# Optimization experiments

Measured on AMD Instinct MI355X. Metric: run time of the kernel, lower is better.

Reference implementation:

```python
import jax, jax.numpy as jnp
import numpy as np

HEAD_DIM = 64
NUM_HEAD = 8
NUM_CLUSTERS = 16
B, N, M = 2, 2048, 2048


def setup_inputs() -> dict:
    key = jax.random.key(0)
    ks = jax.random.split(key, 10)
    d = HEAD_DIM
    inp = {
        "Q": jax.random.normal(ks[0], (B, NUM_HEAD, N, d), jnp.float32),
        "K": jax.random.normal(ks[1], (B, NUM_HEAD, M, d), jnp.float32),
        "V": jax.random.normal(ks[2], (B, NUM_HEAD, M, d), jnp.float32),
        "mask": jnp.zeros((B, M), jnp.int32),
        "noise": jax.random.uniform(ks[3], (B, NUM_HEAD, N, M), jnp.float32),
        "emb": jax.random.normal(ks[4], (NUM_HEAD * NUM_CLUSTERS, d), jnp.float32),
        "W1": jax.random.normal(ks[5], (d, d), jnp.float32) * 0.02,
        "b1": jnp.zeros((d,), jnp.float32),
        "W2": jax.random.normal(ks[6], (d, d), jnp.float32) * 0.02,
        "b2": jnp.zeros((d,), jnp.float32),
        "W3": jax.random.normal(ks[7], (d, d), jnp.float32) * 0.02,
        "b3": jnp.zeros((d,), jnp.float32),
    }
    return inp


def _proj(x, W1, b1, W2, b2, W3, b3):
    # torch nn.Linear: y = x @ W.T + b; dropout is identity in eval mode
    x = jax.nn.relu(jnp.einsum("bhnd,ed->bhne", x, W1) + b1)
    x = jax.nn.relu(jnp.einsum("bhnd,ed->bhne", x, W2) + b2)
    return jnp.einsum("bhnd,ed->bhne", x, W3) + b3


def reference(Q, K, V, mask, noise, emb, W1, b1, W2, b2, W3, b3):
    b, h, n, d = Q.shape
    m = V.shape[2]
    k = NUM_CLUSTERS

    clusters = emb.reshape(h, k, d)                                  # [h,k,d]
    dist = jnp.einsum("hkd,hjd->hkj", clusters, clusters)            # [h,k,k]
    # softmax over the flattened k*k matrix per head
    S = jax.nn.softmax(dist.reshape(h, k * k), axis=-1).reshape(h, k, k)

    Qhat = jax.nn.sigmoid(jnp.einsum("bhnd,hkd->bhnk", _proj(Q, W1, b1, W2, b2, W3, b3), clusters))
    Khat = jax.nn.sigmoid(jnp.einsum("bhmd,hkd->bhmk", _proj(K, W1, b1, W2, b2, W3, b3), clusters))

    SK = jnp.einsum("hkj,bhmj->bhkm", S, Khat)                       # [b,h,k,m]
    expA = jnp.einsum("bhnk,bhkm->bhnm", Qhat, SK)                   # Bernoulli probs in [0,1]

    # SampleGraphSparseGraph: Bernoulli sample with straight-through gradient
    sample = (noise < expA).astype(Q.dtype)
    graph = expA + jax.lax.stop_gradient(sample - expA)

    dot = jnp.einsum("bhnd,bhmd->bhnm", Q, K) / jnp.sqrt(jnp.asarray(d, Q.dtype))
    dot = jnp.where(mask[:, None, None, :] == 1, -jnp.inf, dot)
    p = jax.nn.softmax(dot, axis=-1) * graph
    # F.normalize(p=1): x / max(||x||_1, 1e-12); p is non-negative
    attn = p / jnp.maximum(jnp.sum(p, axis=-1, keepdims=True), 1e-12)

    X = jnp.einsum("bhnm,bhmd->bhnd", attn, V)
    sparsity = jnp.sum(graph, axis=(0, -1, -2)) / (b * n * m)        # [h]
    return X, sparsity, graph, attn
```

## Files before the change

kernel.cpp:

```cpp
#include <hip/hip_runtime.h>


typedef float  f32x4 __attribute__((ext_vector_type(4)));
typedef float  f32x8 __attribute__((ext_vector_type(8)));
typedef double f64x2 __attribute__((ext_vector_type(2)));
typedef __bf16 bf16x8 __attribute__((ext_vector_type(8)));

__device__ __forceinline__ unsigned short f2bf(float f) {
  __bf16 b = (__bf16)f;
  return __builtin_bit_cast(unsigned short, b);
}

__global__ __launch_bounds__(256) void kS(const float* __restrict__ emb,
                                          double* __restrict__ wsS,
                                          float* __restrict__ wsSP) {
  __shared__ double c[16][65];
  __shared__ double red[256];
  const int t = threadIdx.x, h = blockIdx.x;
  if (t == 0) wsSP[h] = 0.f;
  for (int i = t; i < 1024; i += 256) c[i >> 6][i & 63] = (double)emb[(size_t)h * 1024 + i];
  __syncthreads();
  const int k = t >> 4, j = t & 15;
  double acc = 0.0;
  for (int d = 0; d < 64; ++d) acc += c[k][d] * c[j][d];
  red[t] = acc; __syncthreads();
  for (int s = 128; s > 0; s >>= 1) { if (t < s) red[t] = fmax(red[t], red[t + s]); __syncthreads(); }
  const double mx = red[0]; __syncthreads();
  const double e = exp(acc - mx);
  red[t] = e; __syncthreads();
  for (int s = 128; s > 0; s >>= 1) { if (t < s) red[t] += red[t + s]; __syncthreads(); }
  wsS[h * 256 + t] = e / red[0];
}

__global__ __launch_bounds__(256) void kMLP(
    const float* __restrict__ Q, const float* __restrict__ K,
    const float* __restrict__ emb,
    const float* __restrict__ W1, const float* __restrict__ b1,
    const float* __restrict__ W2, const float* __restrict__ b2,
    const float* __restrict__ W3, const float* __restrict__ b3,
    const double* __restrict__ wsS,
    double* __restrict__ QHAT, double* __restrict__ SKT) {
  __shared__ double Xt[64][65];
  __shared__ float  Wl[64][65];
  __shared__ float  bsS[64];
  __shared__ float  cl[16][65];
  __shared__ double kh[64][17];
  __shared__ double Sl[256];

  const int t = threadIdx.x;
  const int blk = blockIdx.x;
  const int side = blk >> 9;
  const int idx = blk & 511;
  const int bh = idx >> 5;
  const int h = bh & 7;
  const int chunk = idx & 31;
  const size_t t0 = (size_t)bh * 2048 + (size_t)chunk * 64;

  const float* src = side ? K : Q;
  for (int i = t; i < 4096; i += 256) Xt[i >> 6][i & 63] = (double)src[t0 * 64 + i];

  const float* Ws[3] = {W1, W2, W3};
  const float* bs[3] = {b1, b2, b3};
  const int te = t & 15, tt = t >> 4;
  const int e0 = te * 4, tok0 = tt * 4;

  for (int l = 0; l < 3; ++l) {
    __syncthreads();
    for (int i = t; i < 4096; i += 256) Wl[i >> 6][i & 63] = Ws[l][i];
    if (t < 64) bsS[t] = bs[l][t];
    __syncthreads();
    double o[4][4];
#pragma unroll
    for (int i = 0; i < 4; ++i)
#pragma unroll
      for (int j = 0; j < 4; ++j) o[i][j] = 0.0;
    for (int d = 0; d < 64; ++d) {
      const double x0 = Xt[tok0 + 0][d], x1 = Xt[tok0 + 1][d], x2 = Xt[tok0 + 2][d], x3 = Xt[tok0 + 3][d];
      const double w0 = (double)Wl[e0 + 0][d], w1 = (double)Wl[e0 + 1][d];
      const double w2 = (double)Wl[e0 + 2][d], w3 = (double)Wl[e0 + 3][d];
      o[0][0] += x0 * w0; o[0][1] += x0 * w1; o[0][2] += x0 * w2; o[0][3] += x0 * w3;
      o[1][0] += x1 * w0; o[1][1] += x1 * w1; o[1][2] += x1 * w2; o[1][3] += x1 * w3;
      o[2][0] += x2 * w0; o[2][1] += x2 * w1; o[2][2] += x2 * w2; o[2][3] += x2 * w3;
      o[3][0] += x3 * w0; o[3][1] += x3 * w1; o[3][2] += x3 * w2; o[3][3] += x3 * w3;
    }
#pragma unroll
    for (int i = 0; i < 4; ++i)
#pragma unroll
      for (int j = 0; j < 4; ++j) {
        double v = o[i][j] + (double)bsS[e0 + j];
        if (l < 2) v = fmax(v, 0.0);
        o[i][j] = v;
      }
    __syncthreads();
#pragma unroll
    for (int i = 0; i < 4; ++i)
#pragma unroll
      for (int j = 0; j < 4; ++j) Xt[tok0 + i][e0 + j] = o[i][j];
  }
  __syncthreads();
  for (int i = t; i < 1024; i += 256) cl[i >> 6][i & 63] = emb[(size_t)h * 1024 + i];
  if (side) { for (int i = t; i < 256; i += 256) Sl[i] = wsS[h * 256 + i]; }
  __syncthreads();

  const int tok = t >> 2, k0 = (t & 3) * 4;
  double z[4] = {0.0, 0.0, 0.0, 0.0};
  for (int d = 0; d < 64; ++d) {
    const double xv = Xt[tok][d];
    z[0] += xv * (double)cl[k0 + 0][d]; z[1] += xv * (double)cl[k0 + 1][d];
    z[2] += xv * (double)cl[k0 + 2][d]; z[3] += xv * (double)cl[k0 + 3][d];
  }
  double hat[4];
#pragma unroll
  for (int j = 0; j < 4; ++j) hat[j] = 1.0 / (1.0 + exp(-z[j]));

  if (!side) {
#pragma unroll
    for (int j = 0; j < 4; ++j) QHAT[(t0 + tok) * 16 + k0 + j] = hat[j];
  } else {
    kh[tok][k0 + 0] = hat[0]; kh[tok][k0 + 1] = hat[1];
    kh[tok][k0 + 2] = hat[2]; kh[tok][k0 + 3] = hat[3];
    __syncthreads();
    double sk[4] = {0.0, 0.0, 0.0, 0.0};
    for (int jj = 0; jj < 16; ++jj) {
      const double kv = kh[tok][jj];
      sk[0] += Sl[(k0 + 0) * 16 + jj] * kv; sk[1] += Sl[(k0 + 1) * 16 + jj] * kv;
      sk[2] += Sl[(k0 + 2) * 16 + jj] * kv; sk[3] += Sl[(k0 + 3) * 16 + jj] * kv;
    }
#pragma unroll
    for (int j = 0; j < 4; ++j) SKT[(t0 + tok) * 16 + k0 + j] = sk[j];
  }
}

__global__ __launch_bounds__(256) void kSample(
    const float* __restrict__ noise,
    const double* __restrict__ qhat, const double* __restrict__ skt,
    float* __restrict__ wsSP,
    unsigned long long* __restrict__ GB64, float* __restrict__ GOUT) {
  const int t = threadIdx.x;
  const int lane = t & 63, wave = t >> 6;
  const int nt = blockIdx.x;
  const int mt = blockIdx.y;
  const int bh = blockIdx.z, h = bh & 7;
  const int n0 = nt * 64;
  const int mA = mt * 512 + wave * 64 + lane;
  const int mB = mA + 256;

  double skvA[16], skvB[16];
  {
    const double* spA = skt + ((size_t)bh * 2048 + mA) * 16;
    const double* spB = skt + ((size_t)bh * 2048 + mB) * 16;
#pragma unroll
    for (int q = 0; q < 8; ++q) {
      *(f64x2*)(skvA + 2 * q) = *(const f64x2*)(spA + 2 * q);
      *(f64x2*)(skvB + 2 * q) = *(const f64x2*)(spB + 2 * q);
    }
  }

  const double* qbase = qhat + ((size_t)bh * 2048 + n0) * 16;
  const float* nzbase = noise + ((size_t)bh * 2048 + n0) * 2048;
  float* gobase = GOUT + ((size_t)bh * 2048 + n0) * 2048;
  unsigned long long* gbbase = GB64 + ((size_t)bh * 2048 + n0) * 32;
  const int gA = mA >> 6, gB = mB >> 6;

  int cnt = 0;
  for (int n = 0; n < 64; ++n) {
    const double* qr = qbase + (size_t)n * 16;
    double ea0 = 0.0, ea1 = 0.0;
#pragma unroll
    for (int k = 0; k < 16; ++k) {
      const double qk = qr[k];
      ea0 += qk * skvA[k];
      ea1 += qk * skvB[k];
    }
    const float nzA = nzbase[(size_t)n * 2048 + mA];
    const float nzB = nzbase[(size_t)n * 2048 + mB];
    const int g0 = ((double)nzA < ea0) ? 1 : 0;
    const int g1 = ((double)nzB < ea1) ? 1 : 0;
    cnt += g0 + g1;
    const unsigned long long b0 = __ballot(g0);
    const unsigned long long b1 = __ballot(g1);
    if (lane == 0) {
      gbbase[(size_t)n * 32 + gA] = b0;
      gbbase[(size_t)n * 32 + gB] = b1;
    }
    gobase[(size_t)n * 2048 + mA] = g0 ? 1.0f : 0.0f;
    gobase[(size_t)n * 2048 + mB] = g1 ? 1.0f : 0.0f;
  }
  cnt += __shfl_xor(cnt, 1); cnt += __shfl_xor(cnt, 2); cnt += __shfl_xor(cnt, 4);
  cnt += __shfl_xor(cnt, 8); cnt += __shfl_xor(cnt, 16); cnt += __shfl_xor(cnt, 32);
  if (lane == 0) atomicAdd(&wsSP[h], (float)cnt);
}

__global__ __launch_bounds__(256) void kCvt(const float* __restrict__ K,
                                            const float* __restrict__ V,
                                            unsigned short* __restrict__ KB,
                                            unsigned short* __restrict__ VT) {
  __shared__ float vt[128][65];
  const int t = threadIdx.x;
  const int bh = blockIdx.x, ch = blockIdx.y;
  const size_t base = ((size_t)bh * 2048 + ch * 128) * 64;
  for (int i = t; i < 8192; i += 256) {
    KB[base + i] = f2bf(K[base + i]);
    vt[i >> 6][i & 63] = V[base + i];
  }
  __syncthreads();
  const size_t vbase = (size_t)bh * 64 * 2048 + ch * 128;
  for (int i = t; i < 8192; i += 256) {
    const int d = i >> 7, mm = i & 127;
    VT[vbase + (size_t)d * 2048 + mm] = f2bf(vt[mm][d]);
  }
}

__global__ __launch_bounds__(256, 4) void kAttn(
    const float* __restrict__ Q, const int* __restrict__ maskp,
    const unsigned short* __restrict__ KB, const unsigned short* __restrict__ VT,
    const unsigned int* __restrict__ GB32,
    float* __restrict__ XOUT, float* __restrict__ AOUT) {
  __shared__ unsigned int bitsS[16][64];
  __shared__ unsigned short stageS[4][16][32];
  __shared__ float dredS[4][16];
  __shared__ float dinvS[16];
  __shared__ float xredS[16][68];

  const int t = threadIdx.x;
  const int wave = t >> 6, lane = t & 63;
  const int bh = blockIdx.y, b = bh >> 3;
  const int n0 = blockIdx.x * 16;
  const int hi2 = lane >> 4;
  const int hi8 = hi2 << 3;
  const int g4 = hi2 << 2;
  const int lm = lane & 15;

  for (int i = t; i < 1024; i += 256)
    bitsS[i >> 6][i & 63] = GB32[((size_t)bh * 2048 + n0 + (i >> 6)) * 64 + (i & 63)];
  for (int i = t; i < 16 * 68; i += 256) ((float*)xredS)[i] = 0.f;

  const float* qrow = Q + ((size_t)bh * 2048 + n0 + lm) * 64;
  bf16x8 aq[2];
#pragma unroll
  for (int hh = 0; hh < 2; ++hh) {
    const int d0 = hi8 + hh * 32;
    const f32x4 qa = *(const f32x4*)(qrow + d0);
    const f32x4 qb = *(const f32x4*)(qrow + d0 + 4);
    bf16x8 v;
    v[0] = (__bf16)qa[0]; v[1] = (__bf16)qa[1]; v[2] = (__bf16)qa[2]; v[3] = (__bf16)qa[3];
    v[4] = (__bf16)qb[0]; v[5] = (__bf16)qb[1]; v[6] = (__bf16)qb[2]; v[7] = (__bf16)qb[3];
    aq[hh] = v;
  }

  const unsigned short* kbp = KB + (size_t)bh * 2048 * 64;
  const unsigned short* vtp = VT + (size_t)bh * 64 * 2048;
  const int* mkp = maskp + b * 2048;
  __syncthreads();

  float dsum[4] = {0.f, 0.f, 0.f, 0.f};
  for (int it = 0; it < 16; ++it) {
    const int mb = (wave << 9) + (it << 5);
    f32x4 st[2];
#pragma unroll
    for (int tt = 0; tt < 2; ++tt) {
      const unsigned short* kr = kbp + (size_t)(mb + tt * 16 + lm) * 64 + hi8;
      const bf16x8 b0 = *(const bf16x8*)(kr);
      const bf16x8 b1 = *(const bf16x8*)(kr + 32);
      f32x4 acc = (f32x4){0.f, 0.f, 0.f, 0.f};
      acc = __builtin_amdgcn_mfma_f32_16x16x32_bf16(aq[0], b0, acc, 0, 0, 0);
      acc = __builtin_amdgcn_mfma_f32_16x16x32_bf16(aq[1], b1, acc, 0, 0, 0);
      st[tt] = acc;
    }
#pragma unroll
    for (int tt = 0; tt < 2; ++tt) {
      const int mv = mkp[mb + tt * 16 + lm];
      const f32x4 sv4 = st[tt];
#pragma unroll
      for (int r = 0; r < 4; ++r) {
        const int g = (bitsS[g4 + r][mb >> 5] >> (tt * 16 + lm)) & 1;
        if (g && !mv) dsum[r] += __expf(sv4[r] * 0.125f);
      }
    }
  }
#pragma unroll
  for (int r = 0; r < 4; ++r) {
    float v = dsum[r];
    v += __shfl_xor(v, 1); v += __shfl_xor(v, 2); v += __shfl_xor(v, 4); v += __shfl_xor(v, 8);
    if (lm == 0) dredS[wave][g4 + r] = v;
  }
  __syncthreads();
  if (t < 16) {
    const float dv = dredS[0][t] + dredS[1][t] + dredS[2][t] + dredS[3][t];
    dinvS[t] = 1.0f / fmaxf(dv, 1e-12f);
  }
  __syncthreads();

  const size_t rowbase = (size_t)bh * 2048 + n0;
  f32x4 xacc[4];
#pragma unroll
  for (int td = 0; td < 4; ++td) xacc[td] = (f32x4){0.f, 0.f, 0.f, 0.f};

  for (int it = 0; it < 16; ++it) {
    const int mb = (wave << 9) + (it << 5);
    f32x4 st[2];
#pragma unroll
    for (int tt = 0; tt < 2; ++tt) {
      const unsigned short* kr = kbp + (size_t)(mb + tt * 16 + lm) * 64 + hi8;
      const bf16x8 b0 = *(const bf16x8*)(kr);
      const bf16x8 b1 = *(const bf16x8*)(kr + 32);
      f32x4 acc = (f32x4){0.f, 0.f, 0.f, 0.f};
      acc = __builtin_amdgcn_mfma_f32_16x16x32_bf16(aq[0], b0, acc, 0, 0, 0);
      acc = __builtin_amdgcn_mfma_f32_16x16x32_bf16(aq[1], b1, acc, 0, 0, 0);
      st[tt] = acc;
    }
#pragma unroll
    for (int tt = 0; tt < 2; ++tt) {
      const int mv = mkp[mb + tt * 16 + lm];
      const f32x4 sv4 = st[tt];
#pragma unroll
      for (int r = 0; r < 4; ++r) {
        const int row = g4 + r;
        const int g = (bitsS[row][mb >> 5] >> (tt * 16 + lm)) & 1;
        const float u = (g && !mv) ? __expf(sv4[r] * 0.125f) : 0.f;
        const int col = tt * 16 + lm;
        stageS[wave][row][col ^ (((row >> 2) & 3) << 3)] = f2bf(u);
      }
    }
    {
      const int rdcol = hi8 ^ (((lm >> 2) & 3) << 3);
      const bf16x8 ua = *(const bf16x8*)&stageS[wave][lm][rdcol];
#pragma unroll
      for (int td = 0; td < 4; ++td) {
        const bf16x8 vb = *(const bf16x8*)(vtp + (size_t)(td * 16 + lm) * 2048 + mb + hi8);
        xacc[td] = __builtin_amdgcn_mfma_f32_16x16x32_bf16(ua, vb, xacc[td], 0, 0, 0);
      }
    }
    {
      const int row = lane >> 2, q = lane & 3;
      const int rc = (q * 8) ^ (((row >> 2) & 3) << 3);
      const unsigned short* up = &stageS[wave][row][rc];
      const float inv = dinvS[row];
      f32x8 av;
#pragma unroll
      for (int j = 0; j < 8; ++j) av[j] = (float)__builtin_bit_cast(__bf16, up[j]) * inv;
      *(f32x8*)(AOUT + (rowbase + row) * 2048 + mb + q * 8) = av;
    }
  }

  for (int w = 0; w < 4; ++w) {
    if (wave == w) {
#pragma unroll
      for (int td = 0; td < 4; ++td)
#pragma unroll
        for (int r = 0; r < 4; ++r) xredS[g4 + r][td * 16 + lm] += xacc[td][r];
    }
    __syncthreads();
  }
  for (int i = t; i < 1024; i += 256) {
    const int nl = i >> 6, d = i & 63;
    XOUT[(rowbase + nl) * 64 + d] = xredS[nl][d] * dinvS[nl];
  }
}

__global__ void kFin(const float* __restrict__ wsSP, float* __restrict__ SPOUT) {
  const int t = threadIdx.x;
  if (t < 8) SPOUT[t] = wsSP[t] * (1.0f / 8388608.0f);
}

extern "C" void kernel_launch(void* const* d_in, const int* in_sizes, int n_in,
                              void* d_out, int out_size, void* d_ws, size_t ws_size,
                              hipStream_t stream) {
  const float* Q = (const float*)d_in[0];
  const float* K = (const float*)d_in[1];
  const float* V = (const float*)d_in[2];
  const int* mask = (const int*)d_in[3];
  const float* noise = (const float*)d_in[4];
  const float* emb = (const float*)d_in[5];
  const float* W1 = (const float*)d_in[6];
  const float* b1 = (const float*)d_in[7];
  const float* W2 = (const float*)d_in[8];
  const float* b2 = (const float*)d_in[9];
  const float* W3 = (const float*)d_in[10];
  const float* b3 = (const float*)d_in[11];

  char* ws = (char*)d_ws;
  double* wsS = (double*)(ws + 0);
  float* wsSP = (float*)(ws + 16384);
  double* QHAT = (double*)(ws + 32768);
  double* SKT  = (double*)(ws + 32768 + 4194304);
  unsigned short* KB = (unsigned short*)(ws + 32768);
  unsigned short* VT = (unsigned short*)(ws + 32768 + 4194304);
  unsigned long long* GB64 = (unsigned long long*)(ws + 32768 + 8388608);
  unsigned int* GB32 = (unsigned int*)(ws + 32768 + 8388608);

  float* out = (float*)d_out;
  float* XOUT = out;
  float* SPOUT = out + 2097152;
  float* GOUT = out + 2097160;
  float* AOUT = out + 69206024;

  kS<<<8, 256, 0, stream>>>(emb, wsS, wsSP);
  kMLP<<<1024, 256, 0, stream>>>(Q, K, emb, W1, b1, W2, b2, W3, b3, wsS, QHAT, SKT);
  kSample<<<dim3(32, 4, 16), 256, 0, stream>>>(noise, QHAT, SKT, wsSP, GB64, GOUT);
  kCvt<<<dim3(16, 16), 256, 0, stream>>>(K, V, KB, VT);
  kAttn<<<dim3(128, 16), 256, 0, stream>>>(Q, mask, KB, VT, GB32, XOUT, AOUT);
  kFin<<<1, 64, 0, stream>>>(wsSP, SPOUT);
}
```

Measured before the change: 512.1 us.

## Fuse attention passes: compute PV in first pass, cache exp tiles in registers

The attention kernel now accumulates the unnormalized P·V product during the first pass that computes row sums, and keeps the bf16 exp values packed in 64 registers. The second pass only replays those cached values to write the normalized attention matrix, so the second QK^T MFMA and exponential recomputation go away. Launch bounds drop from 4 to 2 waves per SIMD so the register cache fits. The MLP kernel also switches to vectorized LDS reads with new padding. The cost is lower occupancy and possible register spills.

```diff
diff --git a/kernel.cpp b/kernel.cpp
--- a/kernel.cpp
+++ b/kernel.cpp
@@ -9,6 +9,9 @@
 __device__ __forceinline__ unsigned short f2bf(float f) {
   __bf16 b = (__bf16)f;
   return __builtin_bit_cast(unsigned short, b);
+}
+__device__ __forceinline__ float bf2f(unsigned short u) {
+  return (float)__builtin_bit_cast(__bf16, u);
 }
 
 __global__ __launch_bounds__(256) void kS(const float* __restrict__ emb,
@@ -40,10 +43,10 @@
     const float* __restrict__ W3, const float* __restrict__ b3,
     const double* __restrict__ wsS,
     double* __restrict__ QHAT, double* __restrict__ SKT) {
-  __shared__ double Xt[64][65];
-  __shared__ float  Wl[64][65];
+  __shared__ double Xt[64][66];
+  __shared__ float  Wl[64][68];
   __shared__ float  bsS[64];
-  __shared__ float  cl[16][65];
+  __shared__ float  cl[16][68];
   __shared__ double kh[64][17];
   __shared__ double Sl[256];
 
@@ -74,14 +77,29 @@
     for (int i = 0; i < 4; ++i)
 #pragma unroll
       for (int j = 0; j < 4; ++j) o[i][j] = 0.0;
-    for (int d = 0; d < 64; ++d) {
-      const double x0 = Xt[tok0 + 0][d], x1 = Xt[tok0 + 1][d], x2 = Xt[tok0 + 2][d], x3 = Xt[tok0 + 3][d];
-      const double w0 = (double)Wl[e0 + 0][d], w1 = (double)Wl[e0 + 1][d];
-      const double w2 = (double)Wl[e0 + 2][d], w3 = (double)Wl[e0 + 3][d];
-      o[0][0] += x0 * w0; o[0][1] += x0 * w1; o[0][2] += x0 * w2; o[0][3] += x0 * w3;
-      o[1][0] += x1 * w0; o[1][1] += x1 * w1; o[1][2] += x1 * w2; o[1][3] += x1 * w3;
-      o[2][0] += x2 * w0; o[2][1] += x2 * w1; o[2][2] += x2 * w2; o[2][3] += x2 * w3;
-      o[3][0] += x3 * w0; o[3][1] += x3 * w1; o[3][2] += x3 * w2; o[3][3] += x3 * w3;
+    for (int d = 0; d < 64; d += 4) {
+      double xa[4][4];
+#pragma unroll
+      for (int i = 0; i < 4; ++i) {
+        const f64x2 lo = *(const f64x2*)&Xt[tok0 + i][d];
+        const f64x2 hi = *(const f64x2*)&Xt[tok0 + i][d + 2];
+        xa[i][0] = lo[0]; xa[i][1] = lo[1]; xa[i][2] = hi[0]; xa[i][3] = hi[1];
+      }
+      float4 wb[4];
+#pragma unroll
+      for (int j = 0; j < 4; ++j) wb[j] = *(const float4*)&Wl[e0 + j][d];
+#pragma unroll
+      for (int dd = 0; dd < 4; ++dd) {
+        const double w0 = (double)((dd == 0) ? wb[0].x : (dd == 1) ? wb[0].y : (dd == 2) ? wb[0].z : wb[0].w);
+        const double w1 = (double)((dd == 0) ? wb[1].x : (dd == 1) ? wb[1].y : (dd == 2) ? wb[1].z : wb[1].w);
+        const double w2 = (double)((dd == 0) ? wb[2].x : (dd == 1) ? wb[2].y : (dd == 2) ? wb[2].z : wb[2].w);
+        const double w3 = (double)((dd == 0) ? wb[3].x : (dd == 1) ? wb[3].y : (dd == 2) ? wb[3].z : wb[3].w);
+#pragma unroll
+        for (int i = 0; i < 4; ++i) {
+          const double xv = xa[i][dd];
+          o[i][0] += xv * w0; o[i][1] += xv * w1; o[i][2] += xv * w2; o[i][3] += xv * w3;
+        }
+      }
     }
 #pragma unroll
     for (int i = 0; i < 4; ++i)
@@ -104,10 +122,16 @@
 
   const int tok = t >> 2, k0 = (t & 3) * 4;
   double z[4] = {0.0, 0.0, 0.0, 0.0};
-  for (int d = 0; d < 64; ++d) {
-    const double xv = Xt[tok][d];
-    z[0] += xv * (double)cl[k0 + 0][d]; z[1] += xv * (double)cl[k0 + 1][d];
-    z[2] += xv * (double)cl[k0 + 2][d]; z[3] += xv * (double)cl[k0 + 3][d];
+  for (int d = 0; d < 64; d += 2) {
+    const f64x2 xv = *(const f64x2*)&Xt[tok][d];
+    const float2 c0 = *(const float2*)&cl[k0 + 0][d];
+    const float2 c1 = *(const float2*)&cl[k0 + 1][d];
+    const float2 c2 = *(const float2*)&cl[k0 + 2][d];
+    const float2 c3 = *(const float2*)&cl[k0 + 3][d];
+    z[0] += xv[0] * (double)c0.x; z[1] += xv[0] * (double)c1.x;
+    z[2] += xv[0] * (double)c2.x; z[3] += xv[0] * (double)c3.x;
+    z[0] += xv[1] * (double)c0.y; z[1] += xv[1] * (double)c1.y;
+    z[2] += xv[1] * (double)c2.y; z[3] += xv[1] * (double)c3.y;
   }
   double hat[4];
 #pragma unroll
@@ -211,7 +235,7 @@
   }
 }
 
-__global__ __launch_bounds__(256, 4) void kAttn(
+__global__ __launch_bounds__(256, 2) void kAttn(
     const float* __restrict__ Q, const int* __restrict__ maskp,
     const unsigned short* __restrict__ KB, const unsigned short* __restrict__ VT,
     const unsigned int* __restrict__ GB32,
@@ -254,6 +278,12 @@
   __syncthreads();
 
   float dsum[4] = {0.f, 0.f, 0.f, 0.f};
+  f32x4 xacc[4];
+#pragma unroll
+  for (int td = 0; td < 4; ++td) xacc[td] = (f32x4){0.f, 0.f, 0.f, 0.f};
+  unsigned int upk[64];
+
+#pragma unroll
   for (int it = 0; it < 16; ++it) {
     const int mb = (wave << 9) + (it << 5);
     f32x4 st[2];
@@ -273,11 +303,28 @@
       const f32x4 sv4 = st[tt];
 #pragma unroll
       for (int r = 0; r < 4; ++r) {
-        const int g = (bitsS[g4 + r][mb >> 5] >> (tt * 16 + lm)) & 1;
-        if (g && !mv) dsum[r] += __expf(sv4[r] * 0.125f);
-      }
-    }
-  }
+        const int row = g4 + r;
+        const int g = (bitsS[row][mb >> 5] >> (tt * 16 + lm)) & 1;
+        const float u = (g && !mv) ? __expf(sv4[r] * 0.125f) : 0.f;
+        dsum[r] += u;
+        const unsigned short ub = f2bf(u);
+        const int slot = it * 4 + tt * 2 + (r >> 1);
+        if (r & 1) upk[slot] |= ((unsigned int)ub) << 16;
+        else       upk[slot] = (unsigned int)ub;
+        stageS[wave][row][(tt * 16 + lm) ^ (((row >> 2) & 3) << 3)] = ub;
+      }
+    }
+    {
+      const int rdcol = hi8 ^ (((lm >> 2) & 3) << 3);
+      const bf16x8 ua = *(const bf16x8*)&stageS[wave][lm][rdcol];
+#pragma unroll
+      for (int td = 0; td < 4; ++td) {
+        const bf16x8 vb = *(const bf16x8*)(vtp + (size_t)(td * 16 + lm) * 2048 + mb + hi8);
+        xacc[td] = __builtin_amdgcn_mfma_f32_16x16x32_bf16(ua, vb, xacc[td], 0, 0, 0);
+      }
+    }
+  }
+
 #pragma unroll
   for (int r = 0; r < 4; ++r) {
     float v = dsum[r];
@@ -292,55 +339,27 @@
   __syncthreads();
 
   const size_t rowbase = (size_t)bh * 2048 + n0;
-  f32x4 xacc[4];
-#pragma unroll
-  for (int td = 0; td < 4; ++td) xacc[td] = (f32x4){0.f, 0.f, 0.f, 0.f};
-
+#pragma unroll
   for (int it = 0; it < 16; ++it) {
     const int mb = (wave << 9) + (it << 5);
-    f32x4 st[2];
-#pragma unroll
-    for (int tt = 0; tt < 2; ++tt) {
-      const unsigned short* kr = kbp + (size_t)(mb + tt * 16 + lm) * 64 + hi8;
-      const bf16x8 b0 = *(const bf16x8*)(kr);
-      const bf16x8 b1 = *(const bf16x8*)(kr + 32);
-      f32x4 acc = (f32x4){0.f, 0.f, 0.f, 0.f};
-      acc = __builtin_amdgcn_mfma_f32_16x16x32_bf16(aq[0], b0, acc, 0, 0, 0);
-      acc = __builtin_amdgcn_mfma_f32_16x16x32_bf16(aq[1], b1, acc, 0, 0, 0);
-      st[tt] = acc;
-    }
-#pragma unroll
-    for (int tt = 0; tt < 2; ++tt) {
-      const int mv = mkp[mb + tt * 16 + lm];
-      const f32x4 sv4 = st[tt];
+#pragma unroll
+    for (int tt = 0; tt < 2; ++tt)
 #pragma unroll
       for (int r = 0; r < 4; ++r) {
         const int row = g4 + r;
-        const int g = (bitsS[row][mb >> 5] >> (tt * 16 + lm)) & 1;
-        const float u = (g && !mv) ? __expf(sv4[r] * 0.125f) : 0.f;
-        const int col = tt * 16 + lm;
-        stageS[wave][row][col ^ (((row >> 2) & 3) << 3)] = f2bf(u);
-      }
-    }
-    {
-      const int rdcol = hi8 ^ (((lm >> 2) & 3) << 3);
-      const bf16x8 ua = *(const bf16x8*)&stageS[wave][lm][rdcol];
-#pragma unroll
-      for (int td = 0; td < 4; ++td) {
-        const bf16x8 vb = *(const bf16x8*)(vtp + (size_t)(td * 16 + lm) * 2048 + mb + hi8);
-        xacc[td] = __builtin_amdgcn_mfma_f32_16x16x32_bf16(ua, vb, xacc[td], 0, 0, 0);
-      }
-    }
-    {
-      const int row = lane >> 2, q = lane & 3;
-      const int rc = (q * 8) ^ (((row >> 2) & 3) << 3);
-      const unsigned short* up = &stageS[wave][row][rc];
-      const float inv = dinvS[row];
-      f32x8 av;
-#pragma unroll
-      for (int j = 0; j < 8; ++j) av[j] = (float)__builtin_bit_cast(__bf16, up[j]) * inv;
-      *(f32x8*)(AOUT + (rowbase + row) * 2048 + mb + q * 8) = av;
-    }
+        const int slot = it * 4 + tt * 2 + (r >> 1);
+        const unsigned short ub =
+            (r & 1) ? (unsigned short)(upk[slot] >> 16) : (unsigned short)(upk[slot] & 0xFFFF);
+        stageS[wave][row][(tt * 16 + lm) ^ (((row >> 2) & 3) << 3)] = ub;
+      }
+    const int row = lane >> 2, q = lane & 3;
+    const int rc = (q * 8) ^ (((row >> 2) & 3) << 3);
+    const unsigned short* up = &stageS[wave][row][rc];
+    const float inv = dinvS[row];
+    f32x8 av;
+#pragma unroll
+    for (int j = 0; j < 8; ++j) av[j] = bf2f(up[j]) * inv;
+    *(f32x8*)(AOUT + (rowbase + row) * 2048 + mb + q * 8) = av;
   }
 
   for (int w = 0; w < 4; ++w) {
```

After: 546.4 us. 6.7% more time.
